# Kernel optimization log

Measured on AMD Instinct MI355X. Metric: run time of the kernel, lower is better.

The kernel has to match this reference:

```python
import jax, jax.numpy as jnp
import numpy as np

GROUPS = 16
EPS = 1e-5


def _gn_sigmoid_branch(y, w1, b1, gamma, beta):
    # y: [b, c, L] -> Conv1d 1x1 -> GroupNorm(16) -> sigmoid
    z = jnp.einsum('bcl,dc->bdl', y, w1) + b1[None, :, None]
    b, c, L = z.shape
    zg = z.reshape(b, GROUPS, c // GROUPS, L)
    mu = zg.mean(axis=(2, 3), keepdims=True)
    var = zg.var(axis=(2, 3), keepdims=True)
    zn = ((zg - mu) * jax.lax.rsqrt(var + EPS)).reshape(b, c, L)
    return jax.nn.sigmoid(zn * gamma[None, :, None] + beta[None, :, None])


def setup_inputs() -> dict:
    key = jax.random.key(0)
    ks = jax.random.split(key, 4)
    b, c, h, w = 8, 256, 64, 64
    x = jax.random.normal(ks[0], (b, c, h, w), dtype=jnp.float32)
    w_qkv = jax.random.normal(ks[1], (3 * c, c), dtype=jnp.float32) * (c ** -0.5)
    w1 = jax.random.normal(ks[2], (c, c), dtype=jnp.float32) * (c ** -0.5)
    b1 = jax.random.normal(ks[3], (c,), dtype=jnp.float32) * 0.02
    gn_gamma = jnp.ones((c,), dtype=jnp.float32)
    gn_beta = jnp.zeros((c,), dtype=jnp.float32)
    return {"x": x, "w_qkv": w_qkv, "w1": w1, "b1": b1,
            "gn_gamma": gn_gamma, "gn_beta": gn_beta}


def reference(x, w_qkv, w1, b1, gn_gamma, gn_beta):
    b, c, h, w = x.shape
    scale = c ** (-0.5)
    # ELA gating branch (conv1x1/GN/sigmoid shared between h- and w-pooled paths)
    x_h = _gn_sigmoid_branch(x.mean(axis=3), w1, b1, gn_gamma, gn_beta)  # [b,c,h]
    x_w = _gn_sigmoid_branch(x.mean(axis=2), w1, b1, gn_gamma, gn_beta)  # [b,c,w]
    ela_out = x * x_h[:, :, :, None] * x_w[:, :, None, :]
    # full spatial self-attention
    qkv = jnp.einsum('bchw,dc->bdhw', x, w_qkv).reshape(b, 3 * c, h * w)
    q, k, v = qkv[:, :c], qkv[:, c:2 * c], qkv[:, 2 * c:]  # each [b,c,hw]
    attn = jax.nn.softmax(jnp.einsum('bcn,bcm->bnm', q, k) * scale, axis=-1)
    softmax_out = jnp.einsum('bnm,bcm->bcn', attn, v).reshape(b, c, h, w)
    return ela_out + softmax_out
```

## Files before the change

### kernel.cpp

```cpp
#include <hip/hip_runtime.h>

typedef __bf16 bf16;
typedef float f32x4 __attribute__((ext_vector_type(4)));
typedef float f32x2 __attribute__((ext_vector_type(2)));
typedef __bf16 bf16x8 __attribute__((ext_vector_type(8)));
typedef __bf16 bf16x4 __attribute__((ext_vector_type(4)));

#define NB 8
#define NC 256
#define NL 64
#define NN 4096

__device__ __forceinline__ void gl_lds16(const bf16* g, bf16* l) {
    __builtin_amdgcn_global_load_lds(
        (const __attribute__((address_space(1))) unsigned int*)g,
        (__attribute__((address_space(3))) unsigned int*)l, 16, 0, 0);
}

__device__ __forceinline__ float fexp2(float x) {
#if __has_builtin(__builtin_amdgcn_exp2f)
    return __builtin_amdgcn_exp2f(x);
#else
    return exp2f(x);
#endif
}

#define QSCALE (0.0625f * 1.44269504f)

__global__ void transpose_kernel(const float* __restrict__ x, bf16* __restrict__ xT,
                                 float* __restrict__ xh) {
    __shared__ __align__(16) bf16 ls[256 * 68];
    int h = blockIdx.x;
    int n0 = h * 64;
    int b = blockIdx.y;
    const float* xp = x + (size_t)b * NC * NN + n0;
    int t = threadIdx.x;
    #pragma unroll
    for (int i = 0; i < 16; ++i) {
        int chunk = t + i * 256;
        int c = chunk >> 4, k4 = (chunk & 15) * 4;
        f32x4 v = *(const f32x4*)(xp + (size_t)c * NN + k4);
        bf16x4 o;
        o[0] = (bf16)v[0]; o[1] = (bf16)v[1]; o[2] = (bf16)v[2]; o[3] = (bf16)v[3];
        *(bf16x4*)&ls[c * 68 + k4] = o;
    }
    __syncthreads();
    bf16* xo = xT + ((size_t)b * NN + n0) * NC;
    #pragma unroll
    for (int i = 0; i < 8; ++i) {
        int chunk = t + i * 256;
        int n = chunk >> 5, c0 = (chunk & 31) * 8;
        bf16x8 o;
        #pragma unroll
        for (int j = 0; j < 8; ++j) o[j] = ls[(c0 + j) * 68 + n];
        *(bf16x8*)(xo + (size_t)n * NC + c0) = o;
    }
    float s = 0.f;
    #pragma unroll 8
    for (int j = 0; j < 64; ++j) s += (float)ls[t * 68 + j];
    xh[((size_t)b * NC + t) * NL + h] = s * (1.f / 64.f);
}

__global__ __launch_bounds__(256) void meansw_cast_kernel(
        const bf16* __restrict__ xT, float* __restrict__ xw,
        const float* __restrict__ w, bf16* __restrict__ wb) {
    int b = blockIdx.y;
    int m = blockIdx.x;
    int t = threadIdx.x;
    if (m >= 64) {
        if (b != 0) return;
        int blk = m - 64;
        #pragma unroll
        for (int jj = 0; jj < 8; ++jj) {
            int i = blk * 8192 + jj * 1024 + t * 4;
            f32x4 v = *(const f32x4*)(w + i);
            bf16x4 o;
            o[0] = (bf16)v[0]; o[1] = (bf16)v[1]; o[2] = (bf16)v[2]; o[3] = (bf16)v[3];
            *(bf16x4*)(wb + i) = o;
        }
        return;
    }
    __shared__ float red[8][256];
    int fix = m;
    int c8 = (t & 31) * 8, g = t >> 5;
    float acc[8] = {0.f, 0.f, 0.f, 0.f, 0.f, 0.f, 0.f, 0.f};
    #pragma unroll
    for (int pass = 0; pass < 8; ++pass) {
        int r = g + pass * 8;
        int n = r * 64 + fix;
        bf16x8 v = *(const bf16x8*)(xT + ((size_t)b * NN + n) * NC + c8);
        #pragma unroll
        for (int j = 0; j < 8; ++j) acc[j] += (float)v[j];
    }
    #pragma unroll
    for (int j = 0; j < 8; ++j) red[g][c8 + j] = acc[j];
    __syncthreads();
    float s = red[0][t] + red[1][t] + red[2][t] + red[3][t]
            + red[4][t] + red[5][t] + red[6][t] + red[7][t];
    xw[((size_t)b * NC + t) * NL + fix] = s * (1.f / 64.f);
}

__global__ void branch_kernel(const float* __restrict__ xh_m, const float* __restrict__ xw_m,
                              const float* __restrict__ w1, const float* __restrict__ b1,
                              const float* __restrict__ gamma, const float* __restrict__ beta,
                              float* __restrict__ x_h, float* __restrict__ x_w) {
    __shared__ float ys[NC * NL];
    int id = blockIdx.x;
    int g = id & 15, br = (id >> 4) & 1, b = id >> 5;
    const float* y = (br ? xw_m : xh_m) + (size_t)b * NC * NL;
    float* outp = (br ? x_w : x_h) + (size_t)b * NC * NL;
    int t = threadIdx.x;
    #pragma unroll
    for (int i = 0; i < 16; ++i) {
        int idx = (t + i * 256) * 4;
        *(f32x4*)&ys[idx] = *(const f32x4*)&y[idx];
    }
    __syncthreads();
    int l = t & 63;
    int dq = __builtin_amdgcn_readfirstlane(t >> 6);
    float z[4];
    #pragma unroll
    for (int k = 0; k < 4; ++k) z[k] = b1[g * 16 + dq + 4 * k];
    for (int c = 0; c < 256; ++c) {
        float yv = ys[c * 64 + l];
        #pragma unroll
        for (int k = 0; k < 4; ++k) z[k] += w1[(g * 16 + dq + 4 * k) * 256 + c] * yv;
    }
    float s1 = z[0] + z[1] + z[2] + z[3];
    float s2 = z[0] * z[0] + z[1] * z[1] + z[2] * z[2] + z[3] * z[3];
    #pragma unroll
    for (int off = 1; off < 64; off <<= 1) {
        s1 += __shfl_xor(s1, off);
        s2 += __shfl_xor(s2, off);
    }
    __syncthreads();
    if (l == 0) { ys[dq * 2] = s1; ys[dq * 2 + 1] = s2; }
    __syncthreads();
    s1 = ys[0] + ys[2] + ys[4] + ys[6];
    s2 = ys[1] + ys[3] + ys[5] + ys[7];
    float mean = s1 * (1.f / 1024.f);
    float var = s2 * (1.f / 1024.f) - mean * mean;
    float rs = rsqrtf(var + 1e-5f);
    #pragma unroll
    for (int k = 0; k < 4; ++k) {
        int d = g * 16 + dq + 4 * k;
        float zn = (z[k] - mean) * rs;
        float tt = zn * gamma[d] + beta[d];
        outp[(size_t)d * NL + l] = 1.f / (1.f + __expf(-tt));
    }
}

__global__ __launch_bounds__(256) void qkv_kernel(
        const bf16* __restrict__ xT, const bf16* __restrict__ wb,
        bf16* __restrict__ Q, bf16* __restrict__ K, bf16* __restrict__ V) {
    __shared__ __align__(16) bf16 wbs[64 * 264];
    int b = blockIdx.x & 7;
    int n0 = (blockIdx.x >> 3) * 64;
    int d0 = blockIdx.y * 64;
    int t = threadIdx.x;
    int wave = t >> 6, lane = t & 63, l15 = lane & 15, quad = lane >> 4;

    const bf16* ap = xT + ((size_t)b * NN + n0 + wave * 16 + l15) * NC + quad * 8;
    bf16x8 a[8];
    #pragma unroll
    for (int kc = 0; kc < 8; ++kc) a[kc] = *(const bf16x8*)(ap + kc * 32);

    {
        int row = t & 63, chunk = t >> 6;
        const bf16* gp = wb + (size_t)(d0 + row) * NC + chunk * 64;
        bf16* lp = &wbs[row * 264 + chunk * 64];
        #pragma unroll
        for (int j = 0; j < 8; ++j)
            *(bf16x8*)(lp + j * 8) = *(const bf16x8*)(gp + j * 8);
    }
    __syncthreads();

    f32x4 acc[4];
    #pragma unroll
    for (int dt = 0; dt < 4; ++dt) acc[dt] = f32x4{0.f, 0.f, 0.f, 0.f};
    #pragma unroll
    for (int kc = 0; kc < 8; ++kc) {
        #pragma unroll
        for (int dt = 0; dt < 4; ++dt) {
            bf16x8 bb = *(const bf16x8*)&wbs[(dt * 16 + l15) * 264 + kc * 32 + quad * 8];
            acc[dt] = __builtin_amdgcn_mfma_f32_16x16x32_bf16(a[kc], bb, acc[dt], 0, 0, 0);
        }
    }
    int nbase = n0 + wave * 16 + quad * 4;
    #pragma unroll
    for (int dt = 0; dt < 4; ++dt) {
        int d = d0 + dt * 16 + l15;
        if (d < 256) {
            #pragma unroll
            for (int r = 0; r < 4; ++r)
                Q[((size_t)b * NN + nbase + r) * NC + d] = (bf16)(acc[dt][r] * QSCALE);
        } else if (d < 512) {
            #pragma unroll
            for (int r = 0; r < 4; ++r)
                K[((size_t)b * NN + nbase + r) * NC + (d - 256)] = (bf16)acc[dt][r];
        } else {
            bf16x4 pv;
            #pragma unroll
            for (int r = 0; r < 4; ++r) pv[r] = (bf16)acc[dt][r];
            *(bf16x4*)(V + ((size_t)b * NC + (d - 512)) * NN + nbase) = pv;
        }
    }
}

__global__ __launch_bounds__(256, 2) void flash_kernel(
        const bf16* __restrict__ Q, const bf16* __restrict__ Kg, const bf16* __restrict__ V,
        bf16* __restrict__ Opart, float* __restrict__ lsum) {
    __shared__ __align__(16) bf16 Ks[2][32 * 256];
    __shared__ __align__(16) bf16 Vs[2][256 * 32];
    __shared__ __align__(16) bf16 Ps[4][32 * 40];
    int id = blockIdx.x;
    int b = id & 7, split = (id >> 3) & 1, qt = id >> 4;
    int n0 = qt * 128;
    int t = threadIdx.x;
    int wave = t >> 6, lane = t & 63, l15 = lane & 15, quad = lane >> 4;

    const bf16* kbase = Kg + (size_t)b * NN * NC;
    const bf16* vbase = V + (size_t)b * NC * NN;

    int krow_l = (wave << 3) + (lane >> 5);
    int kgp = lane & 31;
    int vd_l = (wave << 6) + (lane >> 2);
    int vkp = lane & 3;

    bf16x8 qf[2][8];
    #pragma unroll
    for (int mt = 0; mt < 2; ++mt) {
        const bf16* qp = Q + ((size_t)b * NN + n0 + wave * 32 + mt * 16 + l15) * NC + quad * 8;
        #pragma unroll
        for (int kc = 0; kc < 8; ++kc) qf[mt][kc] = *(const bf16x8*)(qp + kc * 32);
    }

    f32x4 oacc[2][16];
    #pragma unroll
    for (int mt = 0; mt < 2; ++mt)
        #pragma unroll
        for (int dt = 0; dt < 16; ++dt) oacc[mt][dt] = f32x4{0.f, 0.f, 0.f, 0.f};
    float li[2] = {0.f, 0.f};

    auto issue = [&](int kt, int buf) {
        int key0 = (split * 64 + kt) * 32;
        bf16* kdst = &Ks[buf][wave * 2048];
        bf16* vdst = &Vs[buf][wave * 2048];
        #pragma unroll
        for (int i = 0; i < 4; ++i) {
            int krow = krow_l + i * 2;
            gl_lds16(kbase + (size_t)(key0 + krow) * NC + ((kgp ^ (krow & 7)) << 3),
                     kdst + i * 512);
            int vd = vd_l + i * 16;
            gl_lds16(vbase + (size_t)vd * NN + key0 + (((vkp - (vd >> 1)) & 3) << 3),
                     vdst + i * 512);
        }
    };

    issue(0, 0);
    for (int kt = 0; kt < 64; ++kt) {
        int cur = kt & 1;
        __syncthreads();
        if (kt < 63) issue(kt + 1, cur ^ 1);
        const bf16* ks = Ks[cur];
        const bf16* vs = Vs[cur];

        f32x4 s[2][2];
        s[0][0] = f32x4{0.f,0.f,0.f,0.f}; s[0][1] = f32x4{0.f,0.f,0.f,0.f};
        s[1][0] = f32x4{0.f,0.f,0.f,0.f}; s[1][1] = f32x4{0.f,0.f,0.f,0.f};
        #pragma unroll
        for (int kc = 0; kc < 8; ++kc) {
            #pragma unroll
            for (int nt = 0; nt < 2; ++nt) {
                int r = nt * 16 + l15;
                bf16x8 kf = *(const bf16x8*)&ks[r * NC + (((kc * 4 + quad) ^ (r & 7)) << 3)];
                s[0][nt] = __builtin_amdgcn_mfma_f32_16x16x32_bf16(kf, qf[0][kc], s[0][nt], 0, 0, 0);
                s[1][nt] = __builtin_amdgcn_mfma_f32_16x16x32_bf16(kf, qf[1][kc], s[1][nt], 0, 0, 0);
            }
        }

        #pragma unroll
        for (int mt = 0; mt < 2; ++mt) {
            float p0[4], p1[4];
            #pragma unroll
            for (int r = 0; r < 4; ++r) {
                p0[r] = fexp2(s[mt][0][r]);
                p1[r] = fexp2(s[mt][1][r]);
            }
            li[mt] += (p0[0] + p0[1]) + (p0[2] + p0[3])
                    + (p1[0] + p1[1]) + (p1[2] + p1[3]);
            bf16x4 w0, w1;
            #pragma unroll
            for (int r = 0; r < 4; ++r) { w0[r] = (bf16)p0[r]; w1[r] = (bf16)p1[r]; }
            *(bf16x4*)&Ps[wave][(mt * 16 + l15) * 40 + quad * 4] = w0;
            *(bf16x4*)&Ps[wave][(mt * 16 + l15) * 40 + 16 + quad * 4] = w1;
        }
        bf16x8 pf0 = *(const bf16x8*)&Ps[wave][l15 * 40 + quad * 8];
        bf16x8 pf1 = *(const bf16x8*)&Ps[wave][(16 + l15) * 40 + quad * 8];
        #pragma unroll
        for (int dt = 0; dt < 16; ++dt) {
            int d = dt * 16 + l15;
            bf16x8 vf = *(const bf16x8*)&vs[(d << 5) + (((quad + (d >> 1)) & 3) << 3)];
            oacc[0][dt] = __builtin_amdgcn_mfma_f32_16x16x32_bf16(pf0, vf, oacc[0][dt], 0, 0, 0);
            oacc[1][dt] = __builtin_amdgcn_mfma_f32_16x16x32_bf16(pf1, vf, oacc[1][dt], 0, 0, 0);
        }
    }

    bf16* op = Opart + (size_t)(split * NB + b) * NN * NC;
    #pragma unroll
    for (int mt = 0; mt < 2; ++mt) {
        float v = li[mt];
        v += __shfl_xor(v, 16);
        v += __shfl_xor(v, 32);
        if (quad == 0)
            lsum[(size_t)(split * NB + b) * NN + n0 + wave * 32 + mt * 16 + l15] = v;
        int nrow = n0 + wave * 32 + mt * 16 + quad * 4;
        #pragma unroll
        for (int dt = 0; dt < 16; ++dt) {
            #pragma unroll
            for (int r = 0; r < 4; ++r)
                op[(size_t)(nrow + r) * NC + dt * 16 + l15] = (bf16)oacc[mt][dt][r];
        }
    }
}

__global__ __launch_bounds__(256) void combine_kernel(
        const bf16* __restrict__ Opart, const float* __restrict__ lsum,
        const float* __restrict__ x, const float* __restrict__ x_h,
        const float* __restrict__ x_w, float* __restrict__ out) {
    __shared__ float ts[64 * 65];
    int h = blockIdx.x, b = blockIdx.y;
    int n0 = h * 64;
    int t = threadIdx.x;
    const size_t oso = (size_t)NB * NN * NC;
    const size_t lso = (size_t)NB * NN;
    for (int c = 0; c < 4; ++c) {
        int d0 = c * 64;
        if (c) __syncthreads();
        #pragma unroll
        for (int i = 0; i < 4; ++i) {
            int n = i * 16 + (t >> 4);
            int dq = (t & 15) * 4;
            size_t obase = ((size_t)b * NN + n0 + n) * NC + d0 + dq;
            bf16x4 o1 = *(const bf16x4*)(Opart + obase);
            bf16x4 o2 = *(const bf16x4*)(Opart + oso + obase);
            size_t lb = (size_t)b * NN + n0 + n;
            float inv = 1.f / (lsum[lb] + lsum[lso + lb]);
            #pragma unroll
            for (int j = 0; j < 4; ++j)
                ts[(dq + j) * 65 + n] = ((float)o1[j] + (float)o2[j]) * inv;
        }
        __syncthreads();
        #pragma unroll
        for (int i = 0; i < 4; ++i) {
            int dd = i * 16 + (t >> 4);
            int nq = (t & 15) * 4;
            int d = d0 + dd;
            size_t cb = (size_t)b * NC + d;
            f32x4 xv = *(const f32x4*)(x + cb * NN + n0 + nq);
            float xhv = x_h[cb * NL + h];
            f32x4 xwv = *(const f32x4*)(x_w + cb * NL + nq);
            f32x4 o;
            #pragma unroll
            for (int j = 0; j < 4; ++j)
                o[j] = ts[dd * 65 + nq + j] + xv[j] * xhv * xwv[j];
            *(f32x4*)(out + cb * NN + n0 + nq) = o;
        }
    }
}

extern "C" void kernel_launch(void* const* d_in, const int* in_sizes, int n_in,
                              void* d_out, int out_size, void* d_ws, size_t ws_size,
                              hipStream_t stream) {
    const float* x      = (const float*)d_in[0];
    const float* w_qkv  = (const float*)d_in[1];
    const float* w1     = (const float*)d_in[2];
    const float* b1     = (const float*)d_in[3];
    const float* gamma  = (const float*)d_in[4];
    const float* beta   = (const float*)d_in[5];
    float* out = (float*)d_out;

    char* ws = (char*)d_ws;
    bf16*  xT    = (bf16*)(ws);
    bf16*  Qw    = (bf16*)(ws + 16777216);
    bf16*  Kw    = (bf16*)(ws + 33554432);
    bf16*  Vw    = (bf16*)(ws + 50331648);
    bf16*  wb    = (bf16*)(ws + 67108864);
    float* xh_m  = (float*)(ws + 67502080);
    float* xw_m  = (float*)(ws + 68026368);
    float* x_h   = (float*)(ws + 68550656);
    float* x_w   = (float*)(ws + 69074944);
    bf16*  Opart = (bf16*)(ws + 69599232);
    float* lsb   = (float*)(ws + 103153664);

    hipLaunchKernelGGL(transpose_kernel, dim3(64, 8), dim3(256), 0, stream, x, xT, xh_m);
    hipLaunchKernelGGL(meansw_cast_kernel, dim3(88, 8), dim3(256), 0, stream,
                       xT, xw_m, w_qkv, wb);
    hipLaunchKernelGGL(branch_kernel, dim3(256), dim3(256), 0, stream,
                       xh_m, xw_m, w1, b1, gamma, beta, x_h, x_w);
    hipLaunchKernelGGL(qkv_kernel, dim3(512, 12), dim3(256), 0, stream, xT, wb, Qw, Kw, Vw);
    hipLaunchKernelGGL(flash_kernel, dim3(512), dim3(256), 0, stream,
                       Qw, Kw, Vw, Opart, lsb);
    hipLaunchKernelGGL(combine_kernel, dim3(64, 8), dim3(256), 0, stream,
                       Opart, lsb, x, x_h, x_w, out);
}
```

Measured before the change: 312.6 us.

## Give each flash wave 64 query rows and store normalized fp16 partials

The flash kernel drops to 128 threads (2 waves), with each wave now holding 64 query rows instead of 32. Each K/V fragment read from LDS therefore feeds four MFMAs instead of two, halving LDS traffic per FLOP. Partial outputs are normalized by their own row sum and stored as fp16 for better precision, and the combine step reweights them by l1/(l1+l2). The cost is much higher register pressure (64 f32x4 accumulators per lane) and fewer waves per block, which can hurt occupancy and latency hiding.

```diff
diff --git a/kernel.cpp b/kernel.cpp
--- a/kernel.cpp
+++ b/kernel.cpp
@@ -2,16 +2,16 @@
 
 typedef __bf16 bf16;
 typedef float f32x4 __attribute__((ext_vector_type(4)));
-typedef float f32x2 __attribute__((ext_vector_type(2)));
 typedef __bf16 bf16x8 __attribute__((ext_vector_type(8)));
 typedef __bf16 bf16x4 __attribute__((ext_vector_type(4)));
+typedef _Float16 f16x4 __attribute__((ext_vector_type(4)));
 
 #define NB 8
 #define NC 256
 #define NL 64
 #define NN 4096
 
-__device__ __forceinline__ void gl_lds16(const bf16* g, bf16* l) {
+__device__ __forceinline__ void gl_lds16(const void* g, void* l) {
     __builtin_amdgcn_global_load_lds(
         (const __attribute__((address_space(1))) unsigned int*)g,
         (__attribute__((address_space(3))) unsigned int*)l, 16, 0, 0);
@@ -207,12 +207,12 @@
     }
 }
 
-__global__ __launch_bounds__(256, 2) void flash_kernel(
+__global__ __launch_bounds__(128, 1) void flash_kernel(
         const bf16* __restrict__ Q, const bf16* __restrict__ Kg, const bf16* __restrict__ V,
-        bf16* __restrict__ Opart, float* __restrict__ lsum) {
+        _Float16* __restrict__ Opart, float* __restrict__ lsum) {
     __shared__ __align__(16) bf16 Ks[2][32 * 256];
     __shared__ __align__(16) bf16 Vs[2][256 * 32];
-    __shared__ __align__(16) bf16 Ps[4][32 * 40];
+    __shared__ __align__(16) bf16 Ps[2][64 * 40];
     int id = blockIdx.x;
     int b = id & 7, split = (id >> 3) & 1, qt = id >> 4;
     int n0 = qt * 128;
@@ -222,38 +222,32 @@
     const bf16* kbase = Kg + (size_t)b * NN * NC;
     const bf16* vbase = V + (size_t)b * NC * NN;
 
-    int krow_l = (wave << 3) + (lane >> 5);
-    int kgp = lane & 31;
-    int vd_l = (wave << 6) + (lane >> 2);
-    int vkp = lane & 3;
-
-    bf16x8 qf[2][8];
-    #pragma unroll
-    for (int mt = 0; mt < 2; ++mt) {
-        const bf16* qp = Q + ((size_t)b * NN + n0 + wave * 32 + mt * 16 + l15) * NC + quad * 8;
+    bf16x8 qf[4][8];
+    #pragma unroll
+    for (int mt = 0; mt < 4; ++mt) {
+        const bf16* qp = Q + ((size_t)b * NN + n0 + wave * 64 + mt * 16 + l15) * NC + quad * 8;
         #pragma unroll
         for (int kc = 0; kc < 8; ++kc) qf[mt][kc] = *(const bf16x8*)(qp + kc * 32);
     }
 
-    f32x4 oacc[2][16];
-    #pragma unroll
-    for (int mt = 0; mt < 2; ++mt)
+    f32x4 oacc[4][16];
+    #pragma unroll
+    for (int mt = 0; mt < 4; ++mt)
         #pragma unroll
         for (int dt = 0; dt < 16; ++dt) oacc[mt][dt] = f32x4{0.f, 0.f, 0.f, 0.f};
-    float li[2] = {0.f, 0.f};
+    float li[4] = {0.f, 0.f, 0.f, 0.f};
 
     auto issue = [&](int kt, int buf) {
         int key0 = (split * 64 + kt) * 32;
-        bf16* kdst = &Ks[buf][wave * 2048];
-        bf16* vdst = &Vs[buf][wave * 2048];
-        #pragma unroll
-        for (int i = 0; i < 4; ++i) {
-            int krow = krow_l + i * 2;
-            gl_lds16(kbase + (size_t)(key0 + krow) * NC + ((kgp ^ (krow & 7)) << 3),
-                     kdst + i * 512);
-            int vd = vd_l + i * 16;
-            gl_lds16(vbase + (size_t)vd * NN + key0 + (((vkp - (vd >> 1)) & 3) << 3),
-                     vdst + i * 512);
+        #pragma unroll
+        for (int i = 0; i < 8; ++i) {
+            int ch = i * 128 + t;
+            int krow = ch >> 5, kcol = ch & 31;
+            gl_lds16(kbase + (size_t)(key0 + krow) * NC + ((kcol ^ (krow & 7)) << 3),
+                     &Ks[buf][(size_t)(i * 128 + wave * 64) * 8]);
+            int vd = ch >> 2, vc = ch & 3;
+            gl_lds16(vbase + (size_t)vd * NN + key0 + (((vc - (vd >> 1)) & 3) << 3),
+                     &Vs[buf][(size_t)(i * 128 + wave * 64) * 8]);
         }
     };
 
@@ -265,22 +259,27 @@
         const bf16* ks = Ks[cur];
         const bf16* vs = Vs[cur];
 
-        f32x4 s[2][2];
-        s[0][0] = f32x4{0.f,0.f,0.f,0.f}; s[0][1] = f32x4{0.f,0.f,0.f,0.f};
-        s[1][0] = f32x4{0.f,0.f,0.f,0.f}; s[1][1] = f32x4{0.f,0.f,0.f,0.f};
+        f32x4 s[4][2];
+        #pragma unroll
+        for (int mt = 0; mt < 4; ++mt) {
+            s[mt][0] = f32x4{0.f, 0.f, 0.f, 0.f};
+            s[mt][1] = f32x4{0.f, 0.f, 0.f, 0.f};
+        }
         #pragma unroll
         for (int kc = 0; kc < 8; ++kc) {
             #pragma unroll
             for (int nt = 0; nt < 2; ++nt) {
                 int r = nt * 16 + l15;
                 bf16x8 kf = *(const bf16x8*)&ks[r * NC + (((kc * 4 + quad) ^ (r & 7)) << 3)];
-                s[0][nt] = __builtin_amdgcn_mfma_f32_16x16x32_bf16(kf, qf[0][kc], s[0][nt], 0, 0, 0);
-                s[1][nt] = __builtin_amdgcn_mfma_f32_16x16x32_bf16(kf, qf[1][kc], s[1][nt], 0, 0, 0);
+                #pragma unroll
+                for (int mt = 0; mt < 4; ++mt)
+                    s[mt][nt] = __builtin_amdgcn_mfma_f32_16x16x32_bf16(
+                                    kf, qf[mt][kc], s[mt][nt], 0, 0, 0);
             }
         }
 
         #pragma unroll
-        for (int mt = 0; mt < 2; ++mt) {
+        for (int mt = 0; mt < 4; ++mt) {
             float p0[4], p1[4];
             #pragma unroll
             for (int r = 0; r < 4; ++r) {
@@ -295,37 +294,46 @@
             *(bf16x4*)&Ps[wave][(mt * 16 + l15) * 40 + quad * 4] = w0;
             *(bf16x4*)&Ps[wave][(mt * 16 + l15) * 40 + 16 + quad * 4] = w1;
         }
-        bf16x8 pf0 = *(const bf16x8*)&Ps[wave][l15 * 40 + quad * 8];
-        bf16x8 pf1 = *(const bf16x8*)&Ps[wave][(16 + l15) * 40 + quad * 8];
+        bf16x8 pf[4];
+        #pragma unroll
+        for (int mt = 0; mt < 4; ++mt)
+            pf[mt] = *(const bf16x8*)&Ps[wave][(mt * 16 + l15) * 40 + quad * 8];
         #pragma unroll
         for (int dt = 0; dt < 16; ++dt) {
             int d = dt * 16 + l15;
             bf16x8 vf = *(const bf16x8*)&vs[(d << 5) + (((quad + (d >> 1)) & 3) << 3)];
-            oacc[0][dt] = __builtin_amdgcn_mfma_f32_16x16x32_bf16(pf0, vf, oacc[0][dt], 0, 0, 0);
-            oacc[1][dt] = __builtin_amdgcn_mfma_f32_16x16x32_bf16(pf1, vf, oacc[1][dt], 0, 0, 0);
-        }
-    }
-
-    bf16* op = Opart + (size_t)(split * NB + b) * NN * NC;
-    #pragma unroll
-    for (int mt = 0; mt < 2; ++mt) {
+            #pragma unroll
+            for (int mt = 0; mt < 4; ++mt)
+                oacc[mt][dt] = __builtin_amdgcn_mfma_f32_16x16x32_bf16(
+                                   pf[mt], vf, oacc[mt][dt], 0, 0, 0);
+        }
+    }
+
+    _Float16* op = Opart + (size_t)(split * NB + b) * NN * NC;
+    #pragma unroll
+    for (int mt = 0; mt < 4; ++mt) {
         float v = li[mt];
         v += __shfl_xor(v, 16);
         v += __shfl_xor(v, 32);
         if (quad == 0)
-            lsum[(size_t)(split * NB + b) * NN + n0 + wave * 32 + mt * 16 + l15] = v;
-        int nrow = n0 + wave * 32 + mt * 16 + quad * 4;
+            lsum[(size_t)(split * NB + b) * NN + n0 + wave * 64 + mt * 16 + l15] = v;
+        float inv[4];
+        #pragma unroll
+        for (int r = 0; r < 4; ++r)
+            inv[r] = 1.f / __shfl(v, quad * 4 + r);
+        int nrow = n0 + wave * 64 + mt * 16 + quad * 4;
         #pragma unroll
         for (int dt = 0; dt < 16; ++dt) {
             #pragma unroll
             for (int r = 0; r < 4; ++r)
-                op[(size_t)(nrow + r) * NC + dt * 16 + l15] = (bf16)oacc[mt][dt][r];
+                op[(size_t)(nrow + r) * NC + dt * 16 + l15] =
+                    (_Float16)(oacc[mt][dt][r] * inv[r]);
         }
     }
 }
 
 __global__ __launch_bounds__(256) void combine_kernel(
-        const bf16* __restrict__ Opart, const float* __restrict__ lsum,
+        const _Float16* __restrict__ Opart, const float* __restrict__ lsum,
         const float* __restrict__ x, const float* __restrict__ x_h,
         const float* __restrict__ x_w, float* __restrict__ out) {
     __shared__ float ts[64 * 65];
@@ -342,13 +350,15 @@
             int n = i * 16 + (t >> 4);
             int dq = (t & 15) * 4;
             size_t obase = ((size_t)b * NN + n0 + n) * NC + d0 + dq;
-            bf16x4 o1 = *(const bf16x4*)(Opart + obase);
-            bf16x4 o2 = *(const bf16x4*)(Opart + oso + obase);
+            f16x4 o1 = *(const f16x4*)(Opart + obase);
+            f16x4 o2 = *(const f16x4*)(Opart + oso + obase);
             size_t lb = (size_t)b * NN + n0 + n;
-            float inv = 1.f / (lsum[lb] + lsum[lso + lb]);
+            float l1 = lsum[lb], l2 = lsum[lso + lb];
+            float inv = 1.f / (l1 + l2);
+            float c1 = l1 * inv, c2 = l2 * inv;
             #pragma unroll
             for (int j = 0; j < 4; ++j)
-                ts[(dq + j) * 65 + n] = ((float)o1[j] + (float)o2[j]) * inv;
+                ts[(dq + j) * 65 + n] = (float)o1[j] * c1 + (float)o2[j] * c2;
         }
         __syncthreads();
         #pragma unroll
@@ -381,17 +391,17 @@
     float* out = (float*)d_out;
 
     char* ws = (char*)d_ws;
-    bf16*  xT    = (bf16*)(ws);
-    bf16*  Qw    = (bf16*)(ws + 16777216);
-    bf16*  Kw    = (bf16*)(ws + 33554432);
-    bf16*  Vw    = (bf16*)(ws + 50331648);
-    bf16*  wb    = (bf16*)(ws + 67108864);
-    float* xh_m  = (float*)(ws + 67502080);
-    float* xw_m  = (float*)(ws + 68026368);
-    float* x_h   = (float*)(ws + 68550656);
-    float* x_w   = (float*)(ws + 69074944);
-    bf16*  Opart = (bf16*)(ws + 69599232);
-    float* lsb   = (float*)(ws + 103153664);
+    bf16*     xT    = (bf16*)(ws);
+    bf16*     Qw    = (bf16*)(ws + 16777216);
+    bf16*     Kw    = (bf16*)(ws + 33554432);
+    bf16*     Vw    = (bf16*)(ws + 50331648);
+    bf16*     wb    = (bf16*)(ws + 67108864);
+    float*    xh_m  = (float*)(ws + 67502080);
+    float*    xw_m  = (float*)(ws + 68026368);
+    float*    x_h   = (float*)(ws + 68550656);
+    float*    x_w   = (float*)(ws + 69074944);
+    _Float16* Opart = (_Float16*)(ws + 69599232);
+    float*    lsb   = (float*)(ws + 103153664);
 
     hipLaunchKernelGGL(transpose_kernel, dim3(64, 8), dim3(256), 0, stream, x, xT, xh_m);
     hipLaunchKernelGGL(meansw_cast_kernel, dim3(88, 8), dim3(256), 0, stream,
@@ -399,7 +409,7 @@
     hipLaunchKernelGGL(branch_kernel, dim3(256), dim3(256), 0, stream,
                        xh_m, xw_m, w1, b1, gamma, beta, x_h, x_w);
     hipLaunchKernelGGL(qkv_kernel, dim3(512, 12), dim3(256), 0, stream, xT, wb, Qw, Kw, Vw);
-    hipLaunchKernelGGL(flash_kernel, dim3(512), dim3(256), 0, stream,
+    hipLaunchKernelGGL(flash_kernel, dim3(512), dim3(128), 0, stream,
                        Qw, Kw, Vw, Opart, lsb);
     hipLaunchKernelGGL(combine_kernel, dim3(64, 8), dim3(256), 0, stream,
                        Opart, lsb, x, x_h, x_w, out);
```

Result: slower. 392.7 us (+25.6%).

## Store normalized attention partials transposed in fp16 and simplify combine kernel

Applied to the files above, without the earlier changes.

The flash kernel now normalizes each split's partial output by its own row sum and writes it in fp16 in a channel-major [d][n] layout. The combine kernel can then read rows contiguously alongside x and out, with no LDS transpose or barriers. It weights the two partials by their sums. This removes the shared-memory transpose pass and makes combine a simple streaming kernel. The cost is extra divides and shuffles in the flash epilogue, and flash stores become strided 8-byte writes across d. The fp16 storage may also change precision compared with bf16.

```diff
diff --git a/kernel.cpp b/kernel.cpp
--- a/kernel.cpp
+++ b/kernel.cpp
@@ -2,16 +2,16 @@
 
 typedef __bf16 bf16;
 typedef float f32x4 __attribute__((ext_vector_type(4)));
-typedef float f32x2 __attribute__((ext_vector_type(2)));
 typedef __bf16 bf16x8 __attribute__((ext_vector_type(8)));
 typedef __bf16 bf16x4 __attribute__((ext_vector_type(4)));
+typedef _Float16 f16x4 __attribute__((ext_vector_type(4)));
 
 #define NB 8
 #define NC 256
 #define NL 64
 #define NN 4096
 
-__device__ __forceinline__ void gl_lds16(const bf16* g, bf16* l) {
+__device__ __forceinline__ void gl_lds16(const void* g, void* l) {
     __builtin_amdgcn_global_load_lds(
         (const __attribute__((address_space(1))) unsigned int*)g,
         (__attribute__((address_space(3))) unsigned int*)l, 16, 0, 0);
@@ -209,7 +209,7 @@
 
 __global__ __launch_bounds__(256, 2) void flash_kernel(
         const bf16* __restrict__ Q, const bf16* __restrict__ Kg, const bf16* __restrict__ V,
-        bf16* __restrict__ Opart, float* __restrict__ lsum) {
+        _Float16* __restrict__ Opart, float* __restrict__ lsum) {
     __shared__ __align__(16) bf16 Ks[2][32 * 256];
     __shared__ __align__(16) bf16 Vs[2][256 * 32];
     __shared__ __align__(16) bf16 Ps[4][32 * 40];
@@ -306,7 +306,7 @@
         }
     }
 
-    bf16* op = Opart + (size_t)(split * NB + b) * NN * NC;
+    _Float16* op = Opart + (size_t)(split * NB + b) * NN * NC;
     #pragma unroll
     for (int mt = 0; mt < 2; ++mt) {
         float v = li[mt];
@@ -314,59 +314,57 @@
         v += __shfl_xor(v, 32);
         if (quad == 0)
             lsum[(size_t)(split * NB + b) * NN + n0 + wave * 32 + mt * 16 + l15] = v;
+        float inv[4];
+        #pragma unroll
+        for (int r = 0; r < 4; ++r)
+            inv[r] = 1.f / __shfl(v, quad * 4 + r);
         int nrow = n0 + wave * 32 + mt * 16 + quad * 4;
         #pragma unroll
         for (int dt = 0; dt < 16; ++dt) {
-            #pragma unroll
-            for (int r = 0; r < 4; ++r)
-                op[(size_t)(nrow + r) * NC + dt * 16 + l15] = (bf16)oacc[mt][dt][r];
+            int d = dt * 16 + l15;
+            f16x4 ov;
+            #pragma unroll
+            for (int r = 0; r < 4; ++r) ov[r] = (_Float16)(oacc[mt][dt][r] * inv[r]);
+            *(f16x4*)(op + (size_t)d * NN + nrow) = ov;
         }
     }
 }
 
 __global__ __launch_bounds__(256) void combine_kernel(
-        const bf16* __restrict__ Opart, const float* __restrict__ lsum,
+        const _Float16* __restrict__ Opart, const float* __restrict__ lsum,
         const float* __restrict__ x, const float* __restrict__ x_h,
         const float* __restrict__ x_w, float* __restrict__ out) {
-    __shared__ float ts[64 * 65];
-    int h = blockIdx.x, b = blockIdx.y;
-    int n0 = h * 64;
+    int id = blockIdx.x;
+    int b = id & 7, d = id >> 3;
     int t = threadIdx.x;
     const size_t oso = (size_t)NB * NN * NC;
     const size_t lso = (size_t)NB * NN;
-    for (int c = 0; c < 4; ++c) {
-        int d0 = c * 64;
-        if (c) __syncthreads();
-        #pragma unroll
-        for (int i = 0; i < 4; ++i) {
-            int n = i * 16 + (t >> 4);
-            int dq = (t & 15) * 4;
-            size_t obase = ((size_t)b * NN + n0 + n) * NC + d0 + dq;
-            bf16x4 o1 = *(const bf16x4*)(Opart + obase);
-            bf16x4 o2 = *(const bf16x4*)(Opart + oso + obase);
-            size_t lb = (size_t)b * NN + n0 + n;
-            float inv = 1.f / (lsum[lb] + lsum[lso + lb]);
-            #pragma unroll
-            for (int j = 0; j < 4; ++j)
-                ts[(dq + j) * 65 + n] = ((float)o1[j] + (float)o2[j]) * inv;
-        }
-        __syncthreads();
-        #pragma unroll
-        for (int i = 0; i < 4; ++i) {
-            int dd = i * 16 + (t >> 4);
-            int nq = (t & 15) * 4;
-            int d = d0 + dd;
-            size_t cb = (size_t)b * NC + d;
-            f32x4 xv = *(const f32x4*)(x + cb * NN + n0 + nq);
-            float xhv = x_h[cb * NL + h];
-            f32x4 xwv = *(const f32x4*)(x_w + cb * NL + nq);
-            f32x4 o;
-            #pragma unroll
-            for (int j = 0; j < 4; ++j)
-                o[j] = ts[dd * 65 + nq + j] + xv[j] * xhv * xwv[j];
-            *(f32x4*)(out + cb * NN + n0 + nq) = o;
-        }
-    }
+    size_t row = ((size_t)b * NC + d) * NN;
+    size_t orow = (size_t)b * NN * NC + (size_t)d * NN;
+    const float* lp = lsum + (size_t)b * NN;
+    float xh = x_h[((size_t)b * NC + d) * NL];
+    const float* xhp = x_h + ((size_t)b * NC + d) * NL;
+    const float* xwp = x_w + ((size_t)b * NC + d) * NL;
+    #pragma unroll
+    for (int i = 0; i < 4; ++i) {
+        int n = i * 1024 + t * 4;
+        f16x4 o1 = *(const f16x4*)(Opart + orow + n);
+        f16x4 o2 = *(const f16x4*)(Opart + oso + orow + n);
+        f32x4 l1 = *(const f32x4*)(lp + n);
+        f32x4 l2 = *(const f32x4*)(lp + lso + n);
+        f32x4 xv = *(const f32x4*)(x + row + n);
+        float xhv = xhp[n >> 6];
+        f32x4 xwv = *(const f32x4*)(xwp + (n & 63));
+        f32x4 o;
+        #pragma unroll
+        for (int j = 0; j < 4; ++j) {
+            float inv = 1.f / (l1[j] + l2[j]);
+            o[j] = ((float)o1[j] * l1[j] + (float)o2[j] * l2[j]) * inv
+                 + xv[j] * xhv * xwv[j];
+        }
+        *(f32x4*)(out + row + n) = o;
+    }
+    (void)xh;
 }
 
 extern "C" void kernel_launch(void* const* d_in, const int* in_sizes, int n_in,
@@ -381,17 +379,17 @@
     float* out = (float*)d_out;
 
     char* ws = (char*)d_ws;
-    bf16*  xT    = (bf16*)(ws);
-    bf16*  Qw    = (bf16*)(ws + 16777216);
-    bf16*  Kw    = (bf16*)(ws + 33554432);
-    bf16*  Vw    = (bf16*)(ws + 50331648);
-    bf16*  wb    = (bf16*)(ws + 67108864);
-    float* xh_m  = (float*)(ws + 67502080);
-    float* xw_m  = (float*)(ws + 68026368);
-    float* x_h   = (float*)(ws + 68550656);
-    float* x_w   = (float*)(ws + 69074944);
-    bf16*  Opart = (bf16*)(ws + 69599232);
-    float* lsb   = (float*)(ws + 103153664);
+    bf16*     xT    = (bf16*)(ws);
+    bf16*     Qw    = (bf16*)(ws + 16777216);
+    bf16*     Kw    = (bf16*)(ws + 33554432);
+    bf16*     Vw    = (bf16*)(ws + 50331648);
+    bf16*     wb    = (bf16*)(ws + 67108864);
+    float*    xh_m  = (float*)(ws + 67502080);
+    float*    xw_m  = (float*)(ws + 68026368);
+    float*    x_h   = (float*)(ws + 68550656);
+    float*    x_w   = (float*)(ws + 69074944);
+    _Float16* Opart = (_Float16*)(ws + 69599232);
+    float*    lsb   = (float*)(ws + 103153664);
 
     hipLaunchKernelGGL(transpose_kernel, dim3(64, 8), dim3(256), 0, stream, x, xT, xh_m);
     hipLaunchKernelGGL(meansw_cast_kernel, dim3(88, 8), dim3(256), 0, stream,
@@ -401,6 +399,6 @@
     hipLaunchKernelGGL(qkv_kernel, dim3(512, 12), dim3(256), 0, stream, xT, wb, Qw, Kw, Vw);
     hipLaunchKernelGGL(flash_kernel, dim3(512), dim3(256), 0, stream,
                        Qw, Kw, Vw, Opart, lsb);
-    hipLaunchKernelGGL(combine_kernel, dim3(64, 8), dim3(256), 0, stream,
+    hipLaunchKernelGGL(combine_kernel, dim3(2048), dim3(256), 0, stream,
                        Opart, lsb, x, x_h, x_w, out);
 }
```

New measurement: 317.5 us. No clear change (+1.6%).
